# Kernel tuning notes

Hardware: AMD Instinct MI355X
Metric: run time of the kernel (lower is better)

Reference implementation:

```python
import jax, jax.numpy as jnp
import numpy as np

B, S, D, H, DFF = 8, 1024, 1024, 16, 4096
DK = D // H
EPS = 1e-5


def setup_inputs() -> dict:
    key = jax.random.key(0)
    ks = jax.random.split(key, 12)
    sc = lambda n: 1.0 / np.sqrt(n)
    return {
        "x": jax.random.normal(ks[0], (B, S, D), jnp.float32),
        "src_mask": jnp.ones((B, 1, 1, S), jnp.int32),
        "wq": jax.random.normal(ks[1], (D, D), jnp.float32) * sc(D),
        "bq": jnp.zeros((D,), jnp.float32),
        "wk": jax.random.normal(ks[2], (D, D), jnp.float32) * sc(D),
        "bk": jnp.zeros((D,), jnp.float32),
        "wv": jax.random.normal(ks[3], (D, D), jnp.float32) * sc(D),
        "bv": jnp.zeros((D,), jnp.float32),
        "wo": jax.random.normal(ks[4], (D, D), jnp.float32) * sc(D),
        "bo": jnp.zeros((D,), jnp.float32),
        "w1": jax.random.normal(ks[5], (DFF, D), jnp.float32) * sc(D),
        "b1": jnp.zeros((DFF,), jnp.float32),
        "w2": jax.random.normal(ks[6], (D, DFF), jnp.float32) * sc(DFF),
        "b2": jnp.zeros((D,), jnp.float32),
        "g1": jnp.ones((1,), jnp.float32),
        "be1": jnp.zeros((1,), jnp.float32),
        "g2": jnp.ones((1,), jnp.float32),
        "be2": jnp.zeros((1,), jnp.float32),
    }


def _layernorm(x, gamma, beta):
    # Faithful to source: torch.var defaults to unbiased (ddof=1); scalar gamma/beta.
    mu = jnp.mean(x, axis=-1, keepdims=True)
    var = jnp.var(x, axis=-1, keepdims=True, ddof=1)
    return gamma * (x - mu) / jnp.sqrt(var + EPS) + beta


def _mha(x, wq, bq, wk, bk, wv, bv, wo, bo):
    q = (x @ wq.T + bq).reshape(B, S, H, DK).transpose(0, 2, 1, 3)
    k = (x @ wk.T + bk).reshape(B, S, H, DK).transpose(0, 2, 1, 3)
    v = (x @ wv.T + bv).reshape(B, S, H, DK).transpose(0, 2, 1, 3)
    scores = jnp.einsum("bhqd,bhkd->bhqk", q, k) / np.sqrt(DK)
    # NOTE: source uses non-inplace masked_fill whose result is discarded,
    # so the mask has no effect on the executed math; we replicate that.
    attn = jax.nn.softmax(scores, axis=-1)
    out = jnp.einsum("bhqk,bhkd->bhqd", attn, v)
    out = out.transpose(0, 2, 1, 3).reshape(B, S, D)
    return out @ wo.T + bo


def reference(x, src_mask, wq, bq, wk, bk, wv, bv, wo, bo,
              w1, b1, w2, b2, g1, be1, g2, be2):
    # residual 1: pre-norm self-attention (dropout=0 in eval)
    x = x + _mha(_layernorm(x, g1, be1), wq, bq, wk, bk, wv, bv, wo, bo)
    # residual 2: pre-norm FFN
    h = _layernorm(x, g2, be2)
    ff = jax.nn.relu(h @ w1.T + b1) @ w2.T + b2
    return x + ff
```

## Files before the change

kernel.cpp:

```cpp
#include <hip/hip_runtime.h>

typedef unsigned short u16;
typedef unsigned int u32;
typedef __attribute__((ext_vector_type(8))) __bf16 bf16x8;
typedef __attribute__((ext_vector_type(4))) float f32x4;

#define B_ 8
#define S_ 1024
#define D_ 1024
#define H_ 16
#define DK_ 64
#define DFF_ 4096
#define LDQKV 3072

__device__ __forceinline__ float bflo(u32 u) { return __uint_as_float(u << 16); }
__device__ __forceinline__ float bfhi(u32 u) { return __uint_as_float(u & 0xffff0000u); }
__device__ __forceinline__ u16 f2bf(float f) {
    u32 u = __float_as_uint(f);
    u += 0x7fffu + ((u >> 16) & 1u);
    return (u16)(u >> 16);
}
__device__ __forceinline__ u32 cvtpk(float lo, float hi) {
    u32 r;
    asm("v_cvt_pk_bf16_f32 %0, %1, %2" : "=v"(r) : "v"(lo), "v"(hi));
    return r;
}

__device__ __forceinline__ void gl2lds16(const u16* g, u16* l) {
    __builtin_amdgcn_global_load_lds(
        (const __attribute__((address_space(1))) void*)g,
        (__attribute__((address_space(3))) void*)l, 16, 0, 0);
}

__global__ __launch_bounds__(256) void sniff_kernel(const u16* __restrict__ w,
                                                    int* __restrict__ flag) {
    float mx = 0.f;
    for (int i = threadIdx.x; i < 4096; i += 256) {
        float v = fabsf(bflo((u32)w[i]));
        if (!isnan(v)) mx = fmaxf(mx, v);
    }
#pragma unroll
    for (int m = 1; m < 64; m <<= 1) mx = fmaxf(mx, __shfl_xor(mx, m, 64));
    __shared__ float wmx[4];
    if ((threadIdx.x & 63) == 0) wmx[threadIdx.x >> 6] = mx;
    __syncthreads();
    if (threadIdx.x == 0) {
        float m2 = fmaxf(fmaxf(wmx[0], wmx[1]), fmaxf(wmx[2], wmx[3]));
        *flag = (m2 > 1e3f) ? 1 : 0;
    }
}

struct BigTbl {
    const void* src[6];
    u16* dst[6];
    int nch[6];
    int total;
};
__global__ __launch_bounds__(256) void norm_big(BigTbl tb,
                                                const int* __restrict__ flag) {
    const int f = *flag;
    for (int idx = blockIdx.x * 256 + threadIdx.x; idx < tb.total;
         idx += gridDim.x * 256) {
        int i = idx, j = 0;
#pragma unroll
        for (int k = 0; k < 5; ++k) {
            if (i >= tb.nch[j]) { i -= tb.nch[j]; ++j; }
        }
        if (f) {
            const float4* s = (const float4*)tb.src[j] + 2 * (size_t)i;
            float4 a = s[0], b = s[1];
            uint4 o;
            o.x = cvtpk(a.x, a.y);
            o.y = cvtpk(a.z, a.w);
            o.z = cvtpk(b.x, b.y);
            o.w = cvtpk(b.z, b.w);
            *((uint4*)tb.dst[j] + i) = o;
        } else {
            *((uint4*)tb.dst[j] + i) = *((const uint4*)tb.src[j] + i);
        }
    }
}

struct SmallTbl {
    const void* src[10];
    u16* dst[10];
    int n[10];
};
__global__ __launch_bounds__(256) void norm_small(SmallTbl tb,
                                                  const int* __restrict__ flag) {
    int i = blockIdx.x * 256 + threadIdx.x;
    const int f = *flag;
#pragma unroll
    for (int j = 0; j < 10; ++j) {
        if (i < tb.n[j]) {
            if (f)
                tb.dst[j][i] = f2bf(((const float*)tb.src[j])[i]);
            else
                tb.dst[j][i] = ((const u16*)tb.src[j])[i];
            return;
        }
        i -= tb.n[j];
    }
}

template <int INF>
__global__ __launch_bounds__(256) void ln_kernel(const void* __restrict__ in,
                                                 const u16* __restrict__ gs,
                                                 const u16* __restrict__ bs,
                                                 u16* __restrict__ out,
                                                 const int* __restrict__ flag) {
    const int row = blockIdx.x, t = threadIdx.x;
    const bool f32in = (INF == 1) || (INF == 2 && flag[0] != 0);
    float v0, v1, v2, v3;
    if (f32in) {
        const float* p = (const float*)in + (size_t)row * D_ + t * 4;
        float4 f = *(const float4*)p;
        v0 = f.x; v1 = f.y; v2 = f.z; v3 = f.w;
    } else {
        const u16* p = (const u16*)in + (size_t)row * D_ + t * 4;
        uint2 u = *(const uint2*)p;
        v0 = bflo(u.x); v1 = bfhi(u.x); v2 = bflo(u.y); v3 = bfhi(u.y);
    }
    float s = v0 + v1 + v2 + v3;
    float sq = v0 * v0 + v1 * v1 + v2 * v2 + v3 * v3;
#pragma unroll
    for (int m = 1; m < 64; m <<= 1) {
        s += __shfl_xor(s, m, 64);
        sq += __shfl_xor(sq, m, 64);
    }
    __shared__ float ss[4], sqs[4];
    const int w = t >> 6;
    if ((t & 63) == 0) { ss[w] = s; sqs[w] = sq; }
    __syncthreads();
    s = ss[0] + ss[1] + ss[2] + ss[3];
    sq = sqs[0] + sqs[1] + sqs[2] + sqs[3];
    const float mu = s * (1.f / 1024.f);
    float var = (sq - 1024.f * mu * mu) * (1.f / 1023.f);
    var = fmaxf(var, 0.f);
    const float rstd = rsqrtf(var + 1e-5f);
    const float gm = bflo((u32)gs[0]);
    const float bt = bflo((u32)bs[0]);
    const float y0 = gm * (v0 - mu) * rstd + bt;
    const float y1 = gm * (v1 - mu) * rstd + bt;
    const float y2 = gm * (v2 - mu) * rstd + bt;
    const float y3 = gm * (v3 - mu) * rstd + bt;
    uint2 uo;
    uo.x = (u32)f2bf(y0) | ((u32)f2bf(y1) << 16);
    uo.y = (u32)f2bf(y2) | ((u32)f2bf(y3) << 16);
    *(uint2*)(out + (size_t)row * D_ + t * 4) = uo;
}

template <int RELU, int RES, int OUTF>
__global__ __launch_bounds__(256, 4) void gemm_bt(const u16* __restrict__ A,
                                                  const u16* __restrict__ W,
                                                  const u16* __restrict__ bias,
                                                  const void* __restrict__ res,
                                                  void* __restrict__ out,
                                                  int M, int N, int K,
                                                  const int* __restrict__ oflag) {
    __shared__ __align__(16) u16 As[128 * 64];
    __shared__ __align__(16) u16 Bs[128 * 64];
    const int t = threadIdx.x;
    const int lane = t & 63, w = t >> 6;
    const int wm = w >> 1, wn = w & 1;

    const int nx = N >> 7;
    const int gsz = nx << 3;
    const int id = blockIdx.x;
    const int grp = id / gsz;
    const int rem = id - grp * gsz;
    const int m0 = ((grp << 3) + (rem & 7)) << 7;
    const int n0 = (rem >> 3) << 7;

    f32x4 acc[4][4];
#pragma unroll
    for (int mi = 0; mi < 4; ++mi)
#pragma unroll
        for (int ni = 0; ni < 4; ++ni) acc[mi][ni] = (f32x4){0.f, 0.f, 0.f, 0.f};

    const int r8 = lane >> 3, s8 = lane & 7;
    const int cg = s8 ^ r8;
    const u16* Ag = A + (size_t)(m0 + w * 8 + r8) * K + cg * 8;
    const u16* Bg = W + (size_t)(n0 + w * 8 + r8) * K + cg * 8;
    const size_t rI = (size_t)32 * K;
    u16* Asd = &As[(w * 8) * 64];
    u16* Bsd = &Bs[(w * 8) * 64];

    const int c = lane & 15, g = lane >> 4;
    const u16* As_r = &As[(wm * 64 + c) * 64];
    const u16* Bs_r = &Bs[(wn * 64 + c) * 64];
    const int sl0 = (g ^ (c & 7)) * 8;
    const int sl1 = ((4 + g) ^ (c & 7)) * 8;

    for (int kt = 0; kt < K; kt += 64) {
        __syncthreads();
        gl2lds16(Ag, Asd);
        gl2lds16(Ag + rI, Asd + 32 * 64);
        gl2lds16(Ag + 2 * rI, Asd + 64 * 64);
        gl2lds16(Ag + 3 * rI, Asd + 96 * 64);
        gl2lds16(Bg, Bsd);
        gl2lds16(Bg + rI, Bsd + 32 * 64);
        gl2lds16(Bg + 2 * rI, Bsd + 64 * 64);
        gl2lds16(Bg + 3 * rI, Bsd + 96 * 64);
        Ag += 64; Bg += 64;
        __syncthreads();
#pragma unroll
        for (int kc = 0; kc < 2; ++kc) {
            const int sl = kc ? sl1 : sl0;
            bf16x8 af[4], bfr[4];
#pragma unroll
            for (int i = 0; i < 4; ++i) {
                af[i] = *(const bf16x8*)(As_r + i * 16 * 64 + sl);
                bfr[i] = *(const bf16x8*)(Bs_r + i * 16 * 64 + sl);
            }
#pragma unroll
            for (int mi = 0; mi < 4; ++mi)
#pragma unroll
                for (int ni = 0; ni < 4; ++ni)
                    acc[mi][ni] = __builtin_amdgcn_mfma_f32_16x16x32_bf16(af[mi], bfr[ni], acc[mi][ni], 0, 0, 0);
        }
    }

    const int fl = oflag ? oflag[0] : 0;
    const bool f32o = (OUTF == 1) || (OUTF == 2 && fl != 0);
    const int qd = lane >> 4, cl = lane & 15;
    float bv[4];
#pragma unroll
    for (int ni = 0; ni < 4; ++ni)
        bv[ni] = bflo((u32)bias[n0 + wn * 64 + ni * 16 + cl]);
#pragma unroll
    for (int mi = 0; mi < 4; ++mi) {
#pragma unroll
        for (int j = 0; j < 4; ++j) {
            const int row = m0 + wm * 64 + mi * 16 + qd * 4 + j;
#pragma unroll
            for (int ni = 0; ni < 4; ++ni) {
                const int col = n0 + wn * 64 + ni * 16 + cl;
                float vv = acc[mi][ni][j] + bv[ni];
                if (RELU) vv = fmaxf(vv, 0.f);
                if (RES == 2) vv += ((const float*)res)[(size_t)row * N + col];
                if (RES == 3) {
                    if (fl)
                        vv += ((const float*)res)[(size_t)row * N + col];
                    else
                        vv += bflo((u32)((const u16*)res)[(size_t)row * N + col]);
                }
                if (f32o)
                    ((float*)out)[(size_t)row * N + col] = vv;
                else
                    ((u16*)out)[(size_t)row * N + col] = f2bf(vv);
            }
        }
    }
}

template <int RELU>
__global__ __launch_bounds__(512, 2) void gemm256(const u16* __restrict__ A,
                                                  const u16* __restrict__ W,
                                                  const u16* __restrict__ bias,
                                                  u16* __restrict__ out,
                                                  int M, int N, int K) {
    __shared__ __align__(16) u16 As[2][2][256 * 32];
    __shared__ __align__(16) u16 Bs[2][2][256 * 32];
    const int t = threadIdx.x;
    const int lane = t & 63, w = t >> 6;
    const int wm = w >> 2, wn = w & 3;

    const int nx = N >> 8;
    const int gsz = nx << 3;
    const int id = blockIdx.x;
    const int grp = id / gsz;
    const int rem = id - grp * gsz;
    const int m0 = ((grp << 3) + (rem & 7)) << 8;
    const int n0 = (rem >> 3) << 8;

    f32x4 acc[8][4];
#pragma unroll
    for (int mi = 0; mi < 8; ++mi)
#pragma unroll
        for (int ni = 0; ni < 4; ++ni) acc[mi][ni] = (f32x4){0.f, 0.f, 0.f, 0.f};

    const int vr = lane >> 2, vs = lane & 3;
    const int cgs = vs ^ ((vr >> 1) & 3);
    const u16* Asrc = A + (size_t)(m0 + w * 16 + vr) * K + cgs * 8;
    const u16* Bsrc = W + (size_t)(n0 + w * 16 + vr) * K + cgs * 8;
    const size_t rI = (size_t)128 * K;

    auto stageA = [&](int p, int kc, int tk) {
        u16* d = &As[p][kc][(w * 16) * 32];
        const u16* s = Asrc + (size_t)tk * 64 + kc * 32;
        gl2lds16(s, d);
        gl2lds16(s + rI, d + 128 * 32);
    };
    auto stageB = [&](int p, int kc, int tk) {
        u16* d = &Bs[p][kc][(w * 16) * 32];
        const u16* s = Bsrc + (size_t)tk * 64 + kc * 32;
        gl2lds16(s, d);
        gl2lds16(s + rI, d + 128 * 32);
    };

    const int c = lane & 15, g = lane >> 4;
    const int sx = (g ^ ((c >> 1) & 3)) << 3;

    const int nt = K >> 6;
    stageA(0, 0, 0); stageB(0, 0, 0);
    stageA(0, 1, 0); stageB(0, 1, 0);
    stageA(1, 0, 1); stageB(1, 0, 1);
    asm volatile("s_waitcnt vmcnt(4)" ::: "memory");
    __builtin_amdgcn_s_barrier();
    __builtin_amdgcn_sched_barrier(0);

    int cur = 0;
    for (int kt = 0; kt < nt; ++kt) {
        {
            bf16x8 af[8], bfv[4];
            const u16* Ab = &As[cur][0][0];
            const u16* Bb = &Bs[cur][0][0];
#pragma unroll
            for (int i = 0; i < 8; ++i)
                af[i] = *(const bf16x8*)(Ab + (wm * 128 + i * 16 + c) * 32 + sx);
#pragma unroll
            for (int i = 0; i < 4; ++i)
                bfv[i] = *(const bf16x8*)(Bb + (wn * 64 + i * 16 + c) * 32 + sx);
            if (kt + 1 < nt) { stageA(cur ^ 1, 1, kt + 1); stageB(cur ^ 1, 1, kt + 1); }
            __builtin_amdgcn_s_barrier();
            __builtin_amdgcn_s_setprio(1);
#pragma unroll
            for (int mi = 0; mi < 8; ++mi)
#pragma unroll
                for (int ni = 0; ni < 4; ++ni)
                    acc[mi][ni] = __builtin_amdgcn_mfma_f32_16x16x32_bf16(
                        af[mi], bfv[ni], acc[mi][ni], 0, 0, 0);
            __builtin_amdgcn_s_setprio(0);
            __builtin_amdgcn_s_barrier();
            __builtin_amdgcn_sched_barrier(0);
        }
        {
            bf16x8 af[8], bfv[4];
            const u16* Ab = &As[cur][1][0];
            const u16* Bb = &Bs[cur][1][0];
#pragma unroll
            for (int i = 0; i < 8; ++i)
                af[i] = *(const bf16x8*)(Ab + (wm * 128 + i * 16 + c) * 32 + sx);
#pragma unroll
            for (int i = 0; i < 4; ++i)
                bfv[i] = *(const bf16x8*)(Bb + (wn * 64 + i * 16 + c) * 32 + sx);
            if (kt + 2 < nt) { stageA(cur, 0, kt + 2); stageB(cur, 0, kt + 2); }
            __builtin_amdgcn_s_barrier();
            __builtin_amdgcn_s_setprio(1);
#pragma unroll
            for (int mi = 0; mi < 8; ++mi)
#pragma unroll
                for (int ni = 0; ni < 4; ++ni)
                    acc[mi][ni] = __builtin_amdgcn_mfma_f32_16x16x32_bf16(
                        af[mi], bfv[ni], acc[mi][ni], 0, 0, 0);
            __builtin_amdgcn_s_setprio(0);
        }
        if (kt < nt - 2)
            asm volatile("s_waitcnt vmcnt(4)" ::: "memory");
        else
            asm volatile("s_waitcnt vmcnt(0)" ::: "memory");
        __builtin_amdgcn_s_barrier();
        __builtin_amdgcn_sched_barrier(0);
        cur ^= 1;
    }

#pragma unroll
    for (int mi = 0; mi < 8; ++mi) {
#pragma unroll
        for (int j = 0; j < 4; ++j) {
            const int row = m0 + wm * 128 + mi * 16 + g * 4 + j;
#pragma unroll
            for (int ni = 0; ni < 4; ++ni) {
                const int col = n0 + wn * 64 + ni * 16 + c;
                float vv = acc[mi][ni][j] + bflo((u32)bias[col]);
                if (RELU) vv = fmaxf(vv, 0.f);
                out[(size_t)row * N + col] = f2bf(vv);
            }
        }
    }
}

__global__ __launch_bounds__(256, 2) void attn_mfma(const u16* __restrict__ QKV,
                                                    u16* __restrict__ O) {
    __shared__ __align__(16) u16 lds[6 * 64 * 64];
    u16* Ks = lds;
    u16* VsT = lds + 64 * 64;

    const int t = threadIdx.x;
    const int lane = t & 63, w = t >> 6;
    u16* Pw = lds + (2 + w) * 64 * 64;
    const int b = blockIdx.y >> 4, h = blockIdx.y & 15;
    const int q_base = blockIdx.x * 256 + w * 64;
    const int c = lane & 15, g = lane >> 4;
    const int c7 = c & 7;
    const float SC = 0.18033688011112042f;

    bf16x8 qfrag[4][2];
#pragma unroll
    for (int ni = 0; ni < 4; ++ni)
#pragma unroll
        for (int kc = 0; kc < 2; ++kc)
            qfrag[ni][kc] = *(const bf16x8*)(QKV + (size_t)(b * S_ + q_base + 16 * ni + c) * LDQKV +
                                             h * 64 + kc * 32 + 8 * g);

    f32x4 acc_o[4][4];
#pragma unroll
    for (int mi = 0; mi < 4; ++mi)
#pragma unroll
        for (int ni = 0; ni < 4; ++ni) acc_o[mi][ni] = (f32x4){0.f, 0.f, 0.f, 0.f};
    float m_st[4] = {-1e30f, -1e30f, -1e30f, -1e30f};
    float l_st[4] = {0.f, 0.f, 0.f, 0.f};

    const size_t kbase = (size_t)(b * S_) * LDQKV + 1024 + h * 64;
    const size_t vbase = (size_t)(b * S_) * LDQKV + 2048 + h * 64;

    const int r8 = lane >> 3, s8 = lane & 7;
    const int cgk = s8 ^ r8;
    const u16* Kg = QKV + kbase + (size_t)(w * 8 + r8) * LDQKV + cgk * 8;
    u16* Ksd = &Ks[(w * 8) * 64];
    const size_t rIk = (size_t)32 * LDQKV;

    const int vr = t >> 3, vdq = t & 7;
    const u16* Vg = QKV + vbase + (size_t)(2 * vr) * LDQKV + vdq * 8;

    int vfx[4];
#pragma unroll
    for (int mi = 0; mi < 4; ++mi) vfx[mi] = c7 ^ ((2 * mi + (c >> 3)) & 7);

    for (int kt = 0; kt < 16; ++kt) {
        __syncthreads();
        gl2lds16(Kg, Ksd);
        gl2lds16(Kg + rIk, Ksd + 32 * 64);
        Kg += (size_t)64 * LDQKV;
        {
            uint4 a = *(const uint4*)Vg;
            uint4 bb = *(const uint4*)(Vg + LDQKV);
            Vg += (size_t)64 * LDQKV;
            const u32 aw[4] = {a.x, a.y, a.z, a.w};
            const u32 bw[4] = {bb.x, bb.y, bb.z, bb.w};
#pragma unroll
            for (int i = 0; i < 8; ++i) {
                u32 wv;
                if (i & 1)
                    wv = (aw[i >> 1] >> 16) | (bw[i >> 1] & 0xffff0000u);
                else
                    wv = (aw[i >> 1] & 0xffffu) | (bw[i >> 1] << 16);
                const int d = vdq * 8 + i;
                *(u32*)&VsT[d * 64 + (((vr >> 2) ^ (i ^ vdq)) << 3) + ((vr & 3) << 1)] = wv;
            }
        }
        __syncthreads();

        f32x4 acc_s[4][4];
#pragma unroll
        for (int mi = 0; mi < 4; ++mi)
#pragma unroll
            for (int ni = 0; ni < 4; ++ni) acc_s[mi][ni] = (f32x4){0.f, 0.f, 0.f, 0.f};
        __builtin_amdgcn_s_setprio(1);
#pragma unroll
        for (int kc = 0; kc < 2; ++kc) {
            bf16x8 kf[4];
#pragma unroll
            for (int mi = 0; mi < 4; ++mi)
                kf[mi] = *(const bf16x8*)&Ks[(16 * mi + c) * 64 + (((kc * 4 + g) ^ c7) << 3)];
#pragma unroll
            for (int mi = 0; mi < 4; ++mi)
#pragma unroll
                for (int ni = 0; ni < 4; ++ni)
                    acc_s[mi][ni] = __builtin_amdgcn_mfma_f32_16x16x32_bf16(
                        kf[mi], qfrag[ni][kc], acc_s[mi][ni], 0, 0, 0);
        }
        __builtin_amdgcn_s_setprio(0);

        float alpha[4];
        bool resc[4];
#pragma unroll
        for (int ni = 0; ni < 4; ++ni) {
            float mx = -1e30f;
#pragma unroll
            for (int mi = 0; mi < 4; ++mi) {
#pragma unroll
                for (int j = 0; j < 4; ++j) mx = fmaxf(mx, acc_s[mi][ni][j]);
            }
            mx = fmaxf(mx, __shfl_xor(mx, 16, 64));
            mx = fmaxf(mx, __shfl_xor(mx, 32, 64));
            const float mo = m_st[ni];
            const float mn = fmaxf(mo, mx);
            resc[ni] = __any(mn > mo);
            if (resc[ni]) {
                alpha[ni] = exp2f((mo - mn) * SC);
                m_st[ni] = mn;
            } else {
                alpha[ni] = 1.f;
            }
            const float nms = m_st[ni] * SC;
            float sum = 0.f;
#pragma unroll
            for (int mi = 0; mi < 4; ++mi) {
                const float p0 = exp2f(fmaf(acc_s[mi][ni][0], SC, -nms));
                const float p1 = exp2f(fmaf(acc_s[mi][ni][1], SC, -nms));
                const float p2 = exp2f(fmaf(acc_s[mi][ni][2], SC, -nms));
                const float p3 = exp2f(fmaf(acc_s[mi][ni][3], SC, -nms));
                sum += (p0 + p1) + (p2 + p3);
                uint2 pk;
                pk.x = cvtpk(p0, p1);
                pk.y = cvtpk(p2, p3);
                *(uint2*)&Pw[(16 * ni + c) * 64 +
                             ((((2 * mi + (g >> 1)) ^ c7) << 3) + ((g & 1) << 2))] = pk;
            }
            sum += __shfl_xor(sum, 16, 64);
            sum += __shfl_xor(sum, 32, 64);
            l_st[ni] = (resc[ni] ? l_st[ni] * alpha[ni] : l_st[ni]) + sum;
        }
#pragma unroll
        for (int ni = 0; ni < 4; ++ni) {
            if (resc[ni]) {
#pragma unroll
                for (int mi = 0; mi < 4; ++mi) {
#pragma unroll
                    for (int j = 0; j < 4; ++j) acc_o[mi][ni][j] *= alpha[ni];
                }
            }
        }

        __builtin_amdgcn_s_setprio(1);
#pragma unroll
        for (int kc = 0; kc < 2; ++kc) {
            bf16x8 vf[4], pf[4];
#pragma unroll
            for (int mi = 0; mi < 4; ++mi)
                vf[mi] = *(const bf16x8*)&VsT[(16 * mi + c) * 64 + (((kc * 4 + g) ^ vfx[mi]) << 3)];
#pragma unroll
            for (int ni = 0; ni < 4; ++ni)
                pf[ni] = *(const bf16x8*)&Pw[(16 * ni + c) * 64 + (((kc * 4 + g) ^ c7) << 3)];
#pragma unroll
            for (int mi = 0; mi < 4; ++mi)
#pragma unroll
                for (int ni = 0; ni < 4; ++ni)
                    acc_o[mi][ni] = __builtin_amdgcn_mfma_f32_16x16x32_bf16(
                        vf[mi], pf[ni], acc_o[mi][ni], 0, 0, 0);
        }
        __builtin_amdgcn_s_setprio(0);
    }

#pragma unroll
    for (int ni = 0; ni < 4; ++ni) {
        const float inv_l = 1.f / l_st[ni];
        u16* op = O + (size_t)(b * S_ + q_base + 16 * ni + c) * D_ + h * 64;
#pragma unroll
        for (int mi = 0; mi < 4; ++mi) {
            uint2 uo;
            uo.x = cvtpk(acc_o[mi][ni][0] * inv_l, acc_o[mi][ni][1] * inv_l);
            uo.y = cvtpk(acc_o[mi][ni][2] * inv_l, acc_o[mi][ni][3] * inv_l);
            *(uint2*)(op + 16 * mi + 4 * g) = uo;
        }
    }
}

extern "C" void kernel_launch(void* const* d_in, const int* in_sizes, int n_in,
                              void* d_out, int out_size, void* d_ws, size_t ws_size,
                              hipStream_t stream) {
    (void)in_sizes; (void)n_in; (void)out_size; (void)ws_size;
    char* ws = (char*)d_ws;
    const size_t MB = 1ull << 20;
    const size_t KB = 1024;
    u16* wqkv = (u16*)(ws + 16 * MB);
    u16* won  = (u16*)(ws + 22 * MB);
    u16* w1n  = (u16*)(ws + 24 * MB);
    u16* w2n  = (u16*)(ws + 32 * MB);
    u16* bqkv = (u16*)(ws + 40 * MB);
    u16* bon  = (u16*)(ws + 40 * MB + 64 * KB);
    u16* b1n  = (u16*)(ws + 40 * MB + 128 * KB);
    u16* b2n  = (u16*)(ws + 40 * MB + 192 * KB);
    u16* g1n  = (u16*)(ws + 40 * MB + 256 * KB);
    u16* be1n = (u16*)(ws + 40 * MB + 320 * KB);
    u16* g2n  = (u16*)(ws + 40 * MB + 384 * KB);
    u16* be2n = (u16*)(ws + 40 * MB + 448 * KB);
    int* flag = (int*)(ws + 40 * MB + 512 * KB);
    u16* h1   = (u16*)(ws + 48 * MB);
    u16* qkv  = (u16*)(ws + 64 * MB);
    float* x2 = (float*)(ws + 64 * MB);
    u16* h2   = (u16*)(ws + 96 * MB);
    u16* f1   = (u16*)(ws + 112 * MB);

    const int M = B_ * S_;

    sniff_kernel<<<1, 256, 0, stream>>>((const u16*)d_in[2], flag);
    {
        BigTbl tb;
        tb.src[0] = d_in[2];  tb.dst[0] = wqkv;               tb.nch[0] = D_ * D_ / 8;
        tb.src[1] = d_in[4];  tb.dst[1] = wqkv + D_ * D_;     tb.nch[1] = D_ * D_ / 8;
        tb.src[2] = d_in[6];  tb.dst[2] = wqkv + 2 * D_ * D_; tb.nch[2] = D_ * D_ / 8;
        tb.src[3] = d_in[8];  tb.dst[3] = won;                tb.nch[3] = D_ * D_ / 8;
        tb.src[4] = d_in[10]; tb.dst[4] = w1n;                tb.nch[4] = DFF_ * D_ / 8;
        tb.src[5] = d_in[12]; tb.dst[5] = w2n;                tb.nch[5] = D_ * DFF_ / 8;
        tb.total = (4 * D_ * D_ + 2 * DFF_ * D_) / 8;
        norm_big<<<2048, 256, 0, stream>>>(tb, flag);
    }
    {
        SmallTbl tb;
        tb.src[0] = d_in[3];  tb.dst[0] = bqkv;          tb.n[0] = D_;
        tb.src[1] = d_in[5];  tb.dst[1] = bqkv + D_;     tb.n[1] = D_;
        tb.src[2] = d_in[7];  tb.dst[2] = bqkv + 2 * D_; tb.n[2] = D_;
        tb.src[3] = d_in[9];  tb.dst[3] = bon;           tb.n[3] = D_;
        tb.src[4] = d_in[11]; tb.dst[4] = b1n;           tb.n[4] = DFF_;
        tb.src[5] = d_in[13]; tb.dst[5] = b2n;           tb.n[5] = D_;
        tb.src[6] = d_in[14]; tb.dst[6] = g1n;           tb.n[6] = 1;
        tb.src[7] = d_in[15]; tb.dst[7] = be1n;          tb.n[7] = 1;
        tb.src[8] = d_in[16]; tb.dst[8] = g2n;           tb.n[8] = 1;
        tb.src[9] = d_in[17]; tb.dst[9] = be2n;          tb.n[9] = 1;
        const int tot = 5 * D_ + DFF_ + 4;
        norm_small<<<(tot + 255) / 256, 256, 0, stream>>>(tb, flag);
    }

    ln_kernel<2><<<M, 256, 0, stream>>>(d_in[0], g1n, be1n, h1, flag);
    gemm256<0><<<(LDQKV / 256) * (M / 256), 512, 0, stream>>>(h1, wqkv, bqkv, qkv, M, LDQKV, D_);
    attn_mfma<<<dim3(S_ / 256, B_ * H_), 256, 0, stream>>>(qkv, h1);
    gemm_bt<0, 3, 1><<<(D_ / 128) * (M / 128), 256, 0, stream>>>(h1, won, bon, d_in[0], x2, M, D_, D_, flag);
    ln_kernel<1><<<M, 256, 0, stream>>>((const void*)x2, g2n, be2n, h2, flag);
    gemm256<1><<<(DFF_ / 256) * (M / 256), 512, 0, stream>>>(h2, w1n, b1n, f1, M, DFF_, D_);
    gemm_bt<0, 2, 2><<<(D_ / 128) * (M / 128), 256, 0, stream>>>(f1, w2n, b2n, (const void*)x2, (void*)d_out, M, D_, DFF_, flag);
}
```

Before: 498.2 us.

## Split GEMM K-loop into four phases with finer-grained staging and waits

Restructures the bf16 GEMM main loop from two half-K blocks into four phases, each loading only half of the A fragments. The global-to-LDS staging of A and B is spread across the phases, and the vmcnt wait is loosened to 8 outstanding loads so that more loads stay in flight. The aim is to overlap memory traffic with MFMA work more evenly and to cut fragment register pressure. The cost is extra workgroup barriers per iteration and a more delicate wait-count invariant.

Result: no change. 506.5 us (+1.7%).

```diff
diff --git a/kernel.cpp b/kernel.cpp
--- a/kernel.cpp
+++ b/kernel.cpp
@@ -306,62 +306,49 @@
     stageA(0, 0, 0); stageB(0, 0, 0);
     stageA(0, 1, 0); stageB(0, 1, 0);
     stageA(1, 0, 1); stageB(1, 0, 1);
-    asm volatile("s_waitcnt vmcnt(4)" ::: "memory");
+    asm volatile("s_waitcnt vmcnt(8)" ::: "memory");
     __builtin_amdgcn_s_barrier();
     __builtin_amdgcn_sched_barrier(0);
 
     int cur = 0;
     for (int kt = 0; kt < nt; ++kt) {
-        {
-            bf16x8 af[8], bfv[4];
-            const u16* Ab = &As[cur][0][0];
-            const u16* Bb = &Bs[cur][0][0];
-#pragma unroll
-            for (int i = 0; i < 8; ++i)
-                af[i] = *(const bf16x8*)(Ab + (wm * 128 + i * 16 + c) * 32 + sx);
+        bf16x8 bfv[4];
+#pragma unroll
+        for (int ph = 0; ph < 4; ++ph) {
+            const int kc = ph >> 1, qm = ph & 1;
+            bf16x8 af[4];
+            const u16* Ab = &As[cur][kc][0];
 #pragma unroll
             for (int i = 0; i < 4; ++i)
-                bfv[i] = *(const bf16x8*)(Bb + (wn * 64 + i * 16 + c) * 32 + sx);
-            if (kt + 1 < nt) { stageA(cur ^ 1, 1, kt + 1); stageB(cur ^ 1, 1, kt + 1); }
+                af[i] = *(const bf16x8*)(Ab + (wm * 128 + (qm * 4 + i) * 16 + c) * 32 + sx);
+            if (qm == 0) {
+                const u16* Bb = &Bs[cur][kc][0];
+#pragma unroll
+                for (int i = 0; i < 4; ++i)
+                    bfv[i] = *(const bf16x8*)(Bb + (wn * 64 + i * 16 + c) * 32 + sx);
+            }
+            if (ph == 0) { if (kt + 1 < nt) stageA(cur ^ 1, 1, kt + 1); }
+            else if (ph == 1) { if (kt + 1 < nt) stageB(cur ^ 1, 1, kt + 1); }
+            else if (ph == 2) { if (kt + 2 < nt) stageA(cur, 0, kt + 2); }
+            else { if (kt + 2 < nt) stageB(cur, 0, kt + 2); }
             __builtin_amdgcn_s_barrier();
             __builtin_amdgcn_s_setprio(1);
 #pragma unroll
-            for (int mi = 0; mi < 8; ++mi)
+            for (int mi = 0; mi < 4; ++mi)
 #pragma unroll
                 for (int ni = 0; ni < 4; ++ni)
-                    acc[mi][ni] = __builtin_amdgcn_mfma_f32_16x16x32_bf16(
-                        af[mi], bfv[ni], acc[mi][ni], 0, 0, 0);
+                    acc[qm * 4 + mi][ni] = __builtin_amdgcn_mfma_f32_16x16x32_bf16(
+                        af[mi], bfv[ni], acc[qm * 4 + mi][ni], 0, 0, 0);
             __builtin_amdgcn_s_setprio(0);
+            if (ph == 1 || ph == 3) {
+                if (kt < nt - 2)
+                    asm volatile("s_waitcnt vmcnt(8)" ::: "memory");
+                else
+                    asm volatile("s_waitcnt vmcnt(0)" ::: "memory");
+            }
             __builtin_amdgcn_s_barrier();
-            __builtin_amdgcn_sched_barrier(0);
-        }
-        {
-            bf16x8 af[8], bfv[4];
-            const u16* Ab = &As[cur][1][0];
-            const u16* Bb = &Bs[cur][1][0];
-#pragma unroll
-            for (int i = 0; i < 8; ++i)
-                af[i] = *(const bf16x8*)(Ab + (wm * 128 + i * 16 + c) * 32 + sx);
-#pragma unroll
-            for (int i = 0; i < 4; ++i)
-                bfv[i] = *(const bf16x8*)(Bb + (wn * 64 + i * 16 + c) * 32 + sx);
-            if (kt + 2 < nt) { stageA(cur, 0, kt + 2); stageB(cur, 0, kt + 2); }
-            __builtin_amdgcn_s_barrier();
-            __builtin_amdgcn_s_setprio(1);
-#pragma unroll
-            for (int mi = 0; mi < 8; ++mi)
-#pragma unroll
-                for (int ni = 0; ni < 4; ++ni)
-                    acc[mi][ni] = __builtin_amdgcn_mfma_f32_16x16x32_bf16(
-                        af[mi], bfv[ni], acc[mi][ni], 0, 0, 0);
-            __builtin_amdgcn_s_setprio(0);
-        }
-        if (kt < nt - 2)
-            asm volatile("s_waitcnt vmcnt(4)" ::: "memory");
-        else
-            asm volatile("s_waitcnt vmcnt(0)" ::: "memory");
-        __builtin_amdgcn_s_barrier();
-        __builtin_amdgcn_sched_barrier(0);
+            if (ph == 1 || ph == 3) __builtin_amdgcn_sched_barrier(0);
+        }
         cur ^= 1;
     }
 
```

## Fuse weight conversion, bias conversion and first layernorm into one prep kernel

Applied to the files above, without the earlier changes.

Removes the runtime dtype sniff kernel and the flag-based branching, assuming fp32 inputs. Merges the large weight conversion, the small bias conversion and the first layernorm into one launch whose blocks split between layernorm rows and conversion chunks. Gamma and beta are now read directly as fp32, and the GEMM epilogues are specialised to fp32 residual and output. This cuts three launches and the per-element flag checks, but drops support for bf16 inputs.

New measurement: 474.9 us. 4.7% less time.

```diff
diff --git a/kernel.cpp b/kernel.cpp
--- a/kernel.cpp
+++ b/kernel.cpp
@@ -14,7 +14,6 @@
 #define LDQKV 3072
 
 __device__ __forceinline__ float bflo(u32 u) { return __uint_as_float(u << 16); }
-__device__ __forceinline__ float bfhi(u32 u) { return __uint_as_float(u & 0xffff0000u); }
 __device__ __forceinline__ u16 f2bf(float f) {
     u32 u = __float_as_uint(f);
     u += 0x7fffu + ((u >> 16) & 1u);
@@ -32,97 +31,74 @@
         (__attribute__((address_space(3))) void*)l, 16, 0, 0);
 }
 
-__global__ __launch_bounds__(256) void sniff_kernel(const u16* __restrict__ w,
-                                                    int* __restrict__ flag) {
-    float mx = 0.f;
-    for (int i = threadIdx.x; i < 4096; i += 256) {
-        float v = fabsf(bflo((u32)w[i]));
-        if (!isnan(v)) mx = fmaxf(mx, v);
-    }
-#pragma unroll
-    for (int m = 1; m < 64; m <<= 1) mx = fmaxf(mx, __shfl_xor(mx, m, 64));
-    __shared__ float wmx[4];
-    if ((threadIdx.x & 63) == 0) wmx[threadIdx.x >> 6] = mx;
-    __syncthreads();
-    if (threadIdx.x == 0) {
-        float m2 = fmaxf(fmaxf(wmx[0], wmx[1]), fmaxf(wmx[2], wmx[3]));
-        *flag = (m2 > 1e3f) ? 1 : 0;
-    }
-}
-
-struct BigTbl {
-    const void* src[6];
-    u16* dst[6];
-    int nch[6];
+struct PrepTbl {
+    const void* src[12];
+    u16* dst[12];
+    int nch[12];
     int total;
+    int convBlocks;
 };
-__global__ __launch_bounds__(256) void norm_big(BigTbl tb,
-                                                const int* __restrict__ flag) {
-    const int f = *flag;
-    for (int idx = blockIdx.x * 256 + threadIdx.x; idx < tb.total;
-         idx += gridDim.x * 256) {
+__global__ __launch_bounds__(256) void prep_kernel(PrepTbl tb,
+                                                   const float* __restrict__ x,
+                                                   const float* __restrict__ g1,
+                                                   const float* __restrict__ be1,
+                                                   u16* __restrict__ ln_out) {
+    const int t = threadIdx.x;
+    if ((int)blockIdx.x < B_ * S_) {
+        const int row = blockIdx.x;
+        const float* p = x + (size_t)row * D_ + t * 4;
+        float4 f = *(const float4*)p;
+        float s = f.x + f.y + f.z + f.w;
+        float sq = f.x * f.x + f.y * f.y + f.z * f.z + f.w * f.w;
+#pragma unroll
+        for (int m = 1; m < 64; m <<= 1) {
+            s += __shfl_xor(s, m, 64);
+            sq += __shfl_xor(sq, m, 64);
+        }
+        __shared__ float ss[4], sqs[4];
+        const int w = t >> 6;
+        if ((t & 63) == 0) { ss[w] = s; sqs[w] = sq; }
+        __syncthreads();
+        s = ss[0] + ss[1] + ss[2] + ss[3];
+        sq = sqs[0] + sqs[1] + sqs[2] + sqs[3];
+        const float mu = s * (1.f / 1024.f);
+        float var = (sq - 1024.f * mu * mu) * (1.f / 1023.f);
+        var = fmaxf(var, 0.f);
+        const float rstd = rsqrtf(var + 1e-5f);
+        const float gm = g1[0], bt = be1[0];
+        uint2 uo;
+        uo.x = cvtpk(gm * (f.x - mu) * rstd + bt, gm * (f.y - mu) * rstd + bt);
+        uo.y = cvtpk(gm * (f.z - mu) * rstd + bt, gm * (f.w - mu) * rstd + bt);
+        *(uint2*)(ln_out + (size_t)row * D_ + t * 4) = uo;
+        return;
+    }
+    const int bid = blockIdx.x - B_ * S_;
+    for (int idx = bid * 256 + t; idx < tb.total; idx += tb.convBlocks * 256) {
         int i = idx, j = 0;
 #pragma unroll
-        for (int k = 0; k < 5; ++k) {
+        for (int k = 0; k < 11; ++k) {
             if (i >= tb.nch[j]) { i -= tb.nch[j]; ++j; }
         }
-        if (f) {
-            const float4* s = (const float4*)tb.src[j] + 2 * (size_t)i;
-            float4 a = s[0], b = s[1];
-            uint4 o;
-            o.x = cvtpk(a.x, a.y);
-            o.y = cvtpk(a.z, a.w);
-            o.z = cvtpk(b.x, b.y);
-            o.w = cvtpk(b.z, b.w);
-            *((uint4*)tb.dst[j] + i) = o;
-        } else {
-            *((uint4*)tb.dst[j] + i) = *((const uint4*)tb.src[j] + i);
-        }
-    }
-}
-
-struct SmallTbl {
-    const void* src[10];
-    u16* dst[10];
-    int n[10];
-};
-__global__ __launch_bounds__(256) void norm_small(SmallTbl tb,
-                                                  const int* __restrict__ flag) {
-    int i = blockIdx.x * 256 + threadIdx.x;
-    const int f = *flag;
-#pragma unroll
-    for (int j = 0; j < 10; ++j) {
-        if (i < tb.n[j]) {
-            if (f)
-                tb.dst[j][i] = f2bf(((const float*)tb.src[j])[i]);
-            else
-                tb.dst[j][i] = ((const u16*)tb.src[j])[i];
-            return;
-        }
-        i -= tb.n[j];
-    }
-}
-
-template <int INF>
-__global__ __launch_bounds__(256) void ln_kernel(const void* __restrict__ in,
-                                                 const u16* __restrict__ gs,
-                                                 const u16* __restrict__ bs,
-                                                 u16* __restrict__ out,
-                                                 const int* __restrict__ flag) {
+        const float4* sp = (const float4*)tb.src[j] + 2 * (size_t)i;
+        float4 a = sp[0], b = sp[1];
+        uint4 o;
+        o.x = cvtpk(a.x, a.y);
+        o.y = cvtpk(a.z, a.w);
+        o.z = cvtpk(b.x, b.y);
+        o.w = cvtpk(b.z, b.w);
+        *((uint4*)tb.dst[j] + i) = o;
+    }
+}
+
+__global__ __launch_bounds__(256) void ln_kernel(const float* __restrict__ in,
+                                                 const float* __restrict__ gs,
+                                                 const float* __restrict__ bs,
+                                                 u16* __restrict__ out) {
     const int row = blockIdx.x, t = threadIdx.x;
-    const bool f32in = (INF == 1) || (INF == 2 && flag[0] != 0);
-    float v0, v1, v2, v3;
-    if (f32in) {
-        const float* p = (const float*)in + (size_t)row * D_ + t * 4;
-        float4 f = *(const float4*)p;
-        v0 = f.x; v1 = f.y; v2 = f.z; v3 = f.w;
-    } else {
-        const u16* p = (const u16*)in + (size_t)row * D_ + t * 4;
-        uint2 u = *(const uint2*)p;
-        v0 = bflo(u.x); v1 = bfhi(u.x); v2 = bflo(u.y); v3 = bfhi(u.y);
-    }
-    float s = v0 + v1 + v2 + v3;
-    float sq = v0 * v0 + v1 * v1 + v2 * v2 + v3 * v3;
+    const float* p = in + (size_t)row * D_ + t * 4;
+    float4 f = *(const float4*)p;
+    float s = f.x + f.y + f.z + f.w;
+    float sq = f.x * f.x + f.y * f.y + f.z * f.z + f.w * f.w;
 #pragma unroll
     for (int m = 1; m < 64; m <<= 1) {
         s += __shfl_xor(s, m, 64);
@@ -138,15 +114,10 @@
     float var = (sq - 1024.f * mu * mu) * (1.f / 1023.f);
     var = fmaxf(var, 0.f);
     const float rstd = rsqrtf(var + 1e-5f);
-    const float gm = bflo((u32)gs[0]);
-    const float bt = bflo((u32)bs[0]);
-    const float y0 = gm * (v0 - mu) * rstd + bt;
-    const float y1 = gm * (v1 - mu) * rstd + bt;
-    const float y2 = gm * (v2 - mu) * rstd + bt;
-    const float y3 = gm * (v3 - mu) * rstd + bt;
+    const float gm = gs[0], bt = bs[0];
     uint2 uo;
-    uo.x = (u32)f2bf(y0) | ((u32)f2bf(y1) << 16);
-    uo.y = (u32)f2bf(y2) | ((u32)f2bf(y3) << 16);
+    uo.x = cvtpk(gm * (f.x - mu) * rstd + bt, gm * (f.y - mu) * rstd + bt);
+    uo.y = cvtpk(gm * (f.z - mu) * rstd + bt, gm * (f.w - mu) * rstd + bt);
     *(uint2*)(out + (size_t)row * D_ + t * 4) = uo;
 }
 
@@ -156,8 +127,7 @@
                                                   const u16* __restrict__ bias,
                                                   const void* __restrict__ res,
                                                   void* __restrict__ out,
-                                                  int M, int N, int K,
-                                                  const int* __restrict__ oflag) {
+                                                  int M, int N, int K) {
     __shared__ __align__(16) u16 As[128 * 64];
     __shared__ __align__(16) u16 Bs[128 * 64];
     const int t = threadIdx.x;
@@ -221,8 +191,6 @@
         }
     }
 
-    const int fl = oflag ? oflag[0] : 0;
-    const bool f32o = (OUTF == 1) || (OUTF == 2 && fl != 0);
     const int qd = lane >> 4, cl = lane & 15;
     float bv[4];
 #pragma unroll
@@ -239,13 +207,7 @@
                 float vv = acc[mi][ni][j] + bv[ni];
                 if (RELU) vv = fmaxf(vv, 0.f);
                 if (RES == 2) vv += ((const float*)res)[(size_t)row * N + col];
-                if (RES == 3) {
-                    if (fl)
-                        vv += ((const float*)res)[(size_t)row * N + col];
-                    else
-                        vv += bflo((u32)((const u16*)res)[(size_t)row * N + col]);
-                }
-                if (f32o)
+                if (OUTF == 1)
                     ((float*)out)[(size_t)row * N + col] = vv;
                 else
                     ((u16*)out)[(size_t)row * N + col] = f2bf(vv);
@@ -573,11 +535,6 @@
     u16* bon  = (u16*)(ws + 40 * MB + 64 * KB);
     u16* b1n  = (u16*)(ws + 40 * MB + 128 * KB);
     u16* b2n  = (u16*)(ws + 40 * MB + 192 * KB);
-    u16* g1n  = (u16*)(ws + 40 * MB + 256 * KB);
-    u16* be1n = (u16*)(ws + 40 * MB + 320 * KB);
-    u16* g2n  = (u16*)(ws + 40 * MB + 384 * KB);
-    u16* be2n = (u16*)(ws + 40 * MB + 448 * KB);
-    int* flag = (int*)(ws + 40 * MB + 512 * KB);
     u16* h1   = (u16*)(ws + 48 * MB);
     u16* qkv  = (u16*)(ws + 64 * MB);
     float* x2 = (float*)(ws + 64 * MB);
@@ -585,40 +542,33 @@
     u16* f1   = (u16*)(ws + 112 * MB);
 
     const int M = B_ * S_;
-
-    sniff_kernel<<<1, 256, 0, stream>>>((const u16*)d_in[2], flag);
+    const int CONV_BLOCKS = 2048;
+
     {
-        BigTbl tb;
-        tb.src[0] = d_in[2];  tb.dst[0] = wqkv;               tb.nch[0] = D_ * D_ / 8;
-        tb.src[1] = d_in[4];  tb.dst[1] = wqkv + D_ * D_;     tb.nch[1] = D_ * D_ / 8;
-        tb.src[2] = d_in[6];  tb.dst[2] = wqkv + 2 * D_ * D_; tb.nch[2] = D_ * D_ / 8;
-        tb.src[3] = d_in[8];  tb.dst[3] = won;                tb.nch[3] = D_ * D_ / 8;
-        tb.src[4] = d_in[10]; tb.dst[4] = w1n;                tb.nch[4] = DFF_ * D_ / 8;
-        tb.src[5] = d_in[12]; tb.dst[5] = w2n;                tb.nch[5] = D_ * DFF_ / 8;
-        tb.total = (4 * D_ * D_ + 2 * DFF_ * D_) / 8;
-        norm_big<<<2048, 256, 0, stream>>>(tb, flag);
-    }
-    {
-        SmallTbl tb;
-        tb.src[0] = d_in[3];  tb.dst[0] = bqkv;          tb.n[0] = D_;
-        tb.src[1] = d_in[5];  tb.dst[1] = bqkv + D_;     tb.n[1] = D_;
-        tb.src[2] = d_in[7];  tb.dst[2] = bqkv + 2 * D_; tb.n[2] = D_;
-        tb.src[3] = d_in[9];  tb.dst[3] = bon;           tb.n[3] = D_;
-        tb.src[4] = d_in[11]; tb.dst[4] = b1n;           tb.n[4] = DFF_;
-        tb.src[5] = d_in[13]; tb.dst[5] = b2n;           tb.n[5] = D_;
-        tb.src[6] = d_in[14]; tb.dst[6] = g1n;           tb.n[6] = 1;
-        tb.src[7] = d_in[15]; tb.dst[7] = be1n;          tb.n[7] = 1;
-        tb.src[8] = d_in[16]; tb.dst[8] = g2n;           tb.n[8] = 1;
-        tb.src[9] = d_in[17]; tb.dst[9] = be2n;          tb.n[9] = 1;
-        const int tot = 5 * D_ + DFF_ + 4;
-        norm_small<<<(tot + 255) / 256, 256, 0, stream>>>(tb, flag);
-    }
-
-    ln_kernel<2><<<M, 256, 0, stream>>>(d_in[0], g1n, be1n, h1, flag);
+        PrepTbl tb;
+        tb.src[0]  = d_in[2];  tb.dst[0]  = wqkv;               tb.nch[0]  = D_ * D_ / 8;
+        tb.src[1]  = d_in[4];  tb.dst[1]  = wqkv + D_ * D_;     tb.nch[1]  = D_ * D_ / 8;
+        tb.src[2]  = d_in[6];  tb.dst[2]  = wqkv + 2 * D_ * D_; tb.nch[2]  = D_ * D_ / 8;
+        tb.src[3]  = d_in[8];  tb.dst[3]  = won;                tb.nch[3]  = D_ * D_ / 8;
+        tb.src[4]  = d_in[10]; tb.dst[4]  = w1n;                tb.nch[4]  = DFF_ * D_ / 8;
+        tb.src[5]  = d_in[12]; tb.dst[5]  = w2n;                tb.nch[5]  = D_ * DFF_ / 8;
+        tb.src[6]  = d_in[3];  tb.dst[6]  = bqkv;               tb.nch[6]  = D_ / 8;
+        tb.src[7]  = d_in[5];  tb.dst[7]  = bqkv + D_;          tb.nch[7]  = D_ / 8;
+        tb.src[8]  = d_in[7];  tb.dst[8]  = bqkv + 2 * D_;      tb.nch[8]  = D_ / 8;
+        tb.src[9]  = d_in[9];  tb.dst[9]  = bon;                tb.nch[9]  = D_ / 8;
+        tb.src[10] = d_in[11]; tb.dst[10] = b1n;                tb.nch[10] = DFF_ / 8;
+        tb.src[11] = d_in[13]; tb.dst[11] = b2n;                tb.nch[11] = D_ / 8;
+        tb.total = (4 * D_ * D_ + 2 * DFF_ * D_ + 5 * D_ + DFF_) / 8;
+        tb.convBlocks = CONV_BLOCKS;
+        prep_kernel<<<M + CONV_BLOCKS, 256, 0, stream>>>(
+            tb, (const float*)d_in[0], (const float*)d_in[14],
+            (const float*)d_in[15], h1);
+    }
+
     gemm256<0><<<(LDQKV / 256) * (M / 256), 512, 0, stream>>>(h1, wqkv, bqkv, qkv, M, LDQKV, D_);
     attn_mfma<<<dim3(S_ / 256, B_ * H_), 256, 0, stream>>>(qkv, h1);
-    gemm_bt<0, 3, 1><<<(D_ / 128) * (M / 128), 256, 0, stream>>>(h1, won, bon, d_in[0], x2, M, D_, D_, flag);
-    ln_kernel<1><<<M, 256, 0, stream>>>((const void*)x2, g2n, be2n, h2, flag);
+    gemm_bt<0, 2, 1><<<(D_ / 128) * (M / 128), 256, 0, stream>>>(h1, won, bon, d_in[0], x2, M, D_, D_);
+    ln_kernel<<<M, 256, 0, stream>>>(x2, (const float*)d_in[16], (const float*)d_in[17], h2);
     gemm256<1><<<(DFF_ / 256) * (M / 256), 512, 0, stream>>>(h2, w1n, b1n, f1, M, DFF_, D_);
-    gemm_bt<0, 2, 2><<<(D_ / 128) * (M / 128), 256, 0, stream>>>(f1, w2n, b2n, (const void*)x2, (void*)d_out, M, D_, DFF_, flag);
-}
+    gemm_bt<0, 2, 1><<<(D_ / 128) * (M / 128), 256, 0, stream>>>(f1, w2n, b2n, x2, d_out, M, D_, DFF_);
+}
```
